# Kernel tuning notes

Hardware: AMD Instinct MI355X
Metric: run time of the kernel (lower is better)

Reference implementation:

```python
import jax, jax.numpy as jnp
import numpy as np

N, E, F, FE, H, R = 100000, 3200000, 2, 7, 64, 500
BN_EPS = 1e-5
LEAKY_SLOPE = 0.01


def _bn(h, g, b):
    # BatchNorm1d in training mode: batch statistics over the node axis
    m = h.mean(0)
    v = h.var(0)
    return (h - m) * jax.lax.rsqrt(v + BN_EPS) * g + b


def _gine_conv(x, src, dst, edge_attr, eps, el_w, el_b, w1, b1, g, bt, w2, b2):
    # message: relu(x_j + Lin(edge_attr)); aggregate: scatter-add at dst
    msg = jax.nn.relu(x[src] + edge_attr @ el_w + el_b)          # [E, d]
    agg = jax.ops.segment_sum(msg, dst, num_segments=N)          # [N, d]
    h = (1.0 + eps) * x + agg
    # nn: Linear -> BN -> ReLU -> Linear -> ReLU
    h = jax.nn.relu(_bn(h @ w1 + b1, g, bt))
    return jax.nn.relu(h @ w2 + b2)


def setup_inputs() -> dict:
    key = jax.random.key(0)
    ks = jax.random.split(key, 16)
    r = lambda k, s, sc=0.1: jax.random.normal(k, s, dtype=jnp.float32) * sc
    return {
        "x": jax.random.normal(ks[0], (N, F), dtype=jnp.float32),
        "edge_attr": jax.random.normal(ks[1], (E, FE), dtype=jnp.float32),
        "edge_index": jax.random.randint(ks[2], (2, E), 0, N),
        "epoch": 1,
        "eps1": jnp.zeros((), jnp.float32),
        "el1_w": r(ks[3], (FE, F)), "el1_b": jnp.zeros((F,), jnp.float32),
        "n1_w1": r(ks[4], (F, H)), "n1_b1": jnp.zeros((H,), jnp.float32),
        "n1_g": jnp.ones((H,), jnp.float32), "n1_bt": jnp.zeros((H,), jnp.float32),
        "n1_w2": r(ks[5], (H, H)), "n1_b2": jnp.zeros((H,), jnp.float32),
        "eps2": jnp.zeros((), jnp.float32),
        "el2_w": r(ks[6], (FE, H)), "el2_b": jnp.zeros((H,), jnp.float32),
        "n2_w1": r(ks[7], (H, H)), "n2_b1": jnp.zeros((H,), jnp.float32),
        "n2_g": jnp.ones((H,), jnp.float32), "n2_bt": jnp.zeros((H,), jnp.float32),
        "n2_w2": r(ks[8], (H, H)), "n2_b2": jnp.zeros((H,), jnp.float32),
        "reg_w": r(ks[9], (H, R)), "reg_b": jnp.zeros((R,), jnp.float32),
        "end_w": r(ks[10], (R, 1)), "end_b": jnp.zeros((1,), jnp.float32),
    }


def reference(x, edge_attr, edge_index, epoch,
              eps1, el1_w, el1_b, n1_w1, n1_b1, n1_g, n1_bt, n1_w2, n1_b2,
              eps2, el2_w, el2_b, n2_w1, n2_b1, n2_g, n2_bt, n2_w2, n2_b2,
              reg_w, reg_b, end_w, end_b):
    src, dst = edge_index[0], edge_index[1]
    out = _gine_conv(x, src, dst, edge_attr, eps1, el1_w, el1_b,
                     n1_w1, n1_b1, n1_g, n1_bt, n1_w2, n1_b2)
    for _ in range(3 - 1):  # num_layers=3, shared conv2 weights
        out = _gine_conv(out, src, dst, edge_attr, eps2, el2_w, el2_b,
                         n2_w1, n2_b1, n2_g, n2_bt, n2_w2, n2_b2)
    # dropout p=0.0 -> identity; epoch only resets dropout, no effect here
    out = out @ reg_w + reg_b
    out = jnp.where(out >= 0, out, LEAKY_SLOPE * out)  # LeakyReLU
    out = out @ end_w + end_b                            # [N, 1]
    return out
```

## Files before the change

kernel.cpp:

```cpp
#include <hip/hip_runtime.h>

#define NN 100000
#define NE 3200000

__global__ __launch_bounds__(256) void count_kernel(const int* __restrict__ dst,
                                                    int* __restrict__ cnt) {
  int stride = gridDim.x * 256;
  for (int e = blockIdx.x * 256 + threadIdx.x; e < NE; e += stride)
    atomicAdd(&cnt[dst[e]], 1);
}

__global__ __launch_bounds__(1024) void scan_kernel(const int* __restrict__ cnt,
                                                    int* __restrict__ rowptr,
                                                    int* __restrict__ ofs) {
  __shared__ int bsum[1024];
  int tid = threadIdx.x;
  const int CH = (NN + 1023) / 1024;
  int lo = tid * CH, hi = lo + CH < NN ? lo + CH : NN;
  if (lo > NN) lo = NN;
  if (hi < lo) hi = lo;
  int s = 0;
  for (int i = lo; i < hi; i++) s += cnt[i];
  bsum[tid] = s;
  __syncthreads();
  for (int off = 1; off < 1024; off <<= 1) {
    int v = bsum[tid];
    int u = (tid >= off) ? bsum[tid - off] : 0;
    __syncthreads();
    bsum[tid] = v + u;
    __syncthreads();
  }
  int pre = (tid == 0) ? 0 : bsum[tid - 1];
  for (int i = lo; i < hi; i++) {
    int cv = cnt[i];
    rowptr[i] = pre;
    ofs[i] = pre;
    pre += cv;
  }
  if (tid == 1023) rowptr[NN] = pre;
}

__global__ __launch_bounds__(256) void scatter2p_kernel(
    const int* __restrict__ src, const int* __restrict__ dst,
    const float* __restrict__ ea, int* __restrict__ ofs,
    float* __restrict__ pe, const float* __restrict__ x,
    const float* __restrict__ elw, const float* __restrict__ elb,
    float* __restrict__ msg1) {
  float w0[7], w1r[7];
#pragma unroll
  for (int k = 0; k < 7; k++) { w0[k] = elw[k * 2]; w1r[k] = elw[k * 2 + 1]; }
  float b0 = elb[0], b1 = elb[1];
  int stride = gridDim.x * 256;
  for (int e = blockIdx.x * 256 + threadIdx.x; e < NE; e += stride) {
    int sn = src[e];
    int pos = atomicAdd(&ofs[dst[e]], 1);
    float av[7];
#pragma unroll
    for (int k = 0; k < 7; k++) av[k] = ea[e * 7 + k];
    float4 a, b;
    a.x = av[0]; a.y = av[1]; a.z = av[2]; a.w = av[3];
    b.x = av[4]; b.y = av[5]; b.z = av[6];
    b.w = __int_as_float(sn);
    ((float4*)pe)[pos * 2 + 0] = a;
    ((float4*)pe)[pos * 2 + 1] = b;
    float m0 = b0, m1 = b1;
#pragma unroll
    for (int k = 0; k < 7; k++) {
      m0 = fmaf(av[k], w0[k], m0);
      m1 = fmaf(av[k], w1r[k], m1);
    }
    m0 = fmaxf(m0 + x[sn * 2 + 0], 0.f);
    m1 = fmaxf(m1 + x[sn * 2 + 1], 0.f);
    float2 mv; mv.x = m0; mv.y = m1;
    ((float2*)msg1)[pos] = mv;
  }
}

__global__ __launch_bounds__(256) void scatter1_kernel(
    const int* __restrict__ dst, int* __restrict__ ofs, int* __restrict__ eid_s) {
  int stride = gridDim.x * 256;
  for (int e = blockIdx.x * 256 + threadIdx.x; e < NE; e += stride) {
    int pos = atomicAdd(&ofs[dst[e]], 1);
    eid_s[pos] = e;
  }
}

__global__ __launch_bounds__(256) void l1sum_kernel(
    const int* __restrict__ rowptr, const float* __restrict__ msg1,
    float* __restrict__ agg) {
  int stride = gridDim.x * 256;
  for (int n = blockIdx.x * 256 + threadIdx.x; n < NN; n += stride) {
    int r0 = rowptr[n], r1 = rowptr[n + 1];
    float a0 = 0.f, a1 = 0.f;
    const float2* mp = (const float2*)msg1;
    for (int i = r0; i < r1; i++) {
      float2 v = mp[i];
      a0 += v.x;
      a1 += v.y;
    }
    agg[n * 2 + 0] = a0;
    agg[n * 2 + 1] = a1;
  }
}

__global__ __launch_bounds__(256) void l1agg_kernel(
    const int* __restrict__ rowptr, const int* __restrict__ eid_s,
    const int* __restrict__ src, const float* __restrict__ ea,
    const float* __restrict__ x, const float* __restrict__ elw,
    const float* __restrict__ elb, float* __restrict__ agg) {
  float w0[7], w1r[7];
#pragma unroll
  for (int k = 0; k < 7; k++) { w0[k] = elw[k * 2]; w1r[k] = elw[k * 2 + 1]; }
  float b0 = elb[0], b1 = elb[1];
  int stride = gridDim.x * 256;
  for (int n = blockIdx.x * 256 + threadIdx.x; n < NN; n += stride) {
    int r0 = rowptr[n], r1 = rowptr[n + 1];
    float a0 = 0.f, a1 = 0.f;
    for (int i = r0; i < r1; i++) {
      int e = eid_s[i];
      int sn = src[e];
      float m0 = b0, m1 = b1;
#pragma unroll
      for (int k = 0; k < 7; k++) {
        float a = ea[e * 7 + k];
        m0 = fmaf(a, w0[k], m0);
        m1 = fmaf(a, w1r[k], m1);
      }
      m0 = fmaxf(m0 + x[sn * 2 + 0], 0.f);
      m1 = fmaxf(m1 + x[sn * 2 + 1], 0.f);
      a0 += m0; a1 += m1;
    }
    agg[n * 2 + 0] = a0;
    agg[n * 2 + 1] = a1;
  }
}

__global__ __launch_bounds__(256) void gine64p_kernel(
    const int* __restrict__ rowptr, const float* __restrict__ edat,
    const float* __restrict__ xin, const float* __restrict__ elw,
    const float* __restrict__ elb, const float* __restrict__ w1,
    const float* __restrict__ b1, const float* __restrict__ eps_p,
    float* __restrict__ tbuf, float* __restrict__ stats) {
  __shared__ float wl[64 * 64];
  __shared__ float hb[4][64];
  __shared__ float red[256];
  int tid = threadIdx.x, lane = tid & 63, wv = tid >> 6;
  for (int i = tid; i < 64 * 64; i += 256) wl[i] = w1[i];
  float wel[7];
#pragma unroll
  for (int k = 0; k < 7; k++) wel[k] = elw[k * 64 + lane];
  float bel = elb[lane], b1c = b1[lane];
  float ep = 1.0f + *eps_p;
  float s = 0.f, ss = 0.f;
  __syncthreads();
  const float4* pe = (const float4*)edat;
  int nw = gridDim.x * 4;
  for (int n = blockIdx.x * 4 + wv; n < NN; n += nw) {
    int r0 = rowptr[n], r1 = rowptr[n + 1];
    float acc = 0.f;
    int i = r0;
    int rem = r1 - r0;
    if (rem >= 4) {
      float4 a0 = pe[2 * i + 0], b0 = pe[2 * i + 1];
      float4 a1 = pe[2 * i + 2], b1v = pe[2 * i + 3];
      float4 a2 = pe[2 * i + 4], b2 = pe[2 * i + 5];
      float4 a3 = pe[2 * i + 6], b3 = pe[2 * i + 7];
      while (true) {
        float g0 = xin[__float_as_int(b0.w) * 64 + lane];
        float g1 = xin[__float_as_int(b1v.w) * 64 + lane];
        float g2 = xin[__float_as_int(b2.w) * 64 + lane];
        float g3 = xin[__float_as_int(b3.w) * 64 + lane];
        i += 4; rem -= 4;
        bool more = rem >= 4;
        int ip = more ? i : r0;
        float4 na0 = pe[2 * ip + 0], nb0 = pe[2 * ip + 1];
        float4 na1 = pe[2 * ip + 2], nb1 = pe[2 * ip + 3];
        float4 na2 = pe[2 * ip + 4], nb2 = pe[2 * ip + 5];
        float4 na3 = pe[2 * ip + 6], nb3 = pe[2 * ip + 7];
        float m0 = bel, m1 = bel, m2 = bel, m3 = bel;
        m0 = fmaf(a0.x, wel[0], m0); m0 = fmaf(a0.y, wel[1], m0);
        m0 = fmaf(a0.z, wel[2], m0); m0 = fmaf(a0.w, wel[3], m0);
        m0 = fmaf(b0.x, wel[4], m0); m0 = fmaf(b0.y, wel[5], m0);
        m0 = fmaf(b0.z, wel[6], m0);
        m1 = fmaf(a1.x, wel[0], m1); m1 = fmaf(a1.y, wel[1], m1);
        m1 = fmaf(a1.z, wel[2], m1); m1 = fmaf(a1.w, wel[3], m1);
        m1 = fmaf(b1v.x, wel[4], m1); m1 = fmaf(b1v.y, wel[5], m1);
        m1 = fmaf(b1v.z, wel[6], m1);
        m2 = fmaf(a2.x, wel[0], m2); m2 = fmaf(a2.y, wel[1], m2);
        m2 = fmaf(a2.z, wel[2], m2); m2 = fmaf(a2.w, wel[3], m2);
        m2 = fmaf(b2.x, wel[4], m2); m2 = fmaf(b2.y, wel[5], m2);
        m2 = fmaf(b2.z, wel[6], m2);
        m3 = fmaf(a3.x, wel[0], m3); m3 = fmaf(a3.y, wel[1], m3);
        m3 = fmaf(a3.z, wel[2], m3); m3 = fmaf(a3.w, wel[3], m3);
        m3 = fmaf(b3.x, wel[4], m3); m3 = fmaf(b3.y, wel[5], m3);
        m3 = fmaf(b3.z, wel[6], m3);
        acc += fmaxf(m0 + g0, 0.f);
        acc += fmaxf(m1 + g1, 0.f);
        acc += fmaxf(m2 + g2, 0.f);
        acc += fmaxf(m3 + g3, 0.f);
        a0 = na0; b0 = nb0; a1 = na1; b1v = nb1;
        a2 = na2; b2 = nb2; a3 = na3; b3 = nb3;
        if (!more) break;
      }
    }
    for (; i < r1; i++) {
      float4 pa = pe[i * 2], pb = pe[i * 2 + 1];
      float m = bel;
      m = fmaf(pa.x, wel[0], m); m = fmaf(pa.y, wel[1], m);
      m = fmaf(pa.z, wel[2], m); m = fmaf(pa.w, wel[3], m);
      m = fmaf(pb.x, wel[4], m); m = fmaf(pb.y, wel[5], m);
      m = fmaf(pb.z, wel[6], m);
      m += xin[__float_as_int(pb.w) * 64 + lane];
      acc += fmaxf(m, 0.f);
    }
    float h = ep * xin[n * 64 + lane] + acc;
    hb[wv][lane] = h;
    float t = b1c;
#pragma unroll
    for (int k = 0; k < 64; k++) t = fmaf(hb[wv][k], wl[k * 64 + lane], t);
    tbuf[n * 64 + lane] = t;
    s += t;
    ss += t * t;
  }
  double* dsum = (double*)stats;
  red[tid] = s;
  __syncthreads();
  if (tid < 64) unsafeAtomicAdd(&dsum[tid], (double)(red[tid] + red[tid + 64] + red[tid + 128] + red[tid + 192]));
  __syncthreads();
  red[tid] = ss;
  __syncthreads();
  if (tid < 64) unsafeAtomicAdd(&dsum[64 + tid], (double)(red[tid] + red[tid + 64] + red[tid + 128] + red[tid + 192]));
}

__global__ __launch_bounds__(256) void gine64s_kernel(
    const int* __restrict__ rowptr, const int* __restrict__ eid_s,
    const int* __restrict__ src, const float* __restrict__ ea,
    const float* __restrict__ xin, const float* __restrict__ elw,
    const float* __restrict__ elb, const float* __restrict__ w1,
    const float* __restrict__ b1, const float* __restrict__ eps_p,
    float* __restrict__ tbuf, float* __restrict__ stats) {
  __shared__ float wl[64 * 64];
  __shared__ float hb[4][64];
  __shared__ float red[256];
  int tid = threadIdx.x, lane = tid & 63, wv = tid >> 6;
  for (int i = tid; i < 64 * 64; i += 256) wl[i] = w1[i];
  float wel[7];
#pragma unroll
  for (int k = 0; k < 7; k++) wel[k] = elw[k * 64 + lane];
  float bel = elb[lane], b1c = b1[lane];
  float ep = 1.0f + *eps_p;
  float s = 0.f, ss = 0.f;
  __syncthreads();
  int nw = gridDim.x * 4;
  for (int n = blockIdx.x * 4 + wv; n < NN; n += nw) {
    int r0 = rowptr[n], r1 = rowptr[n + 1];
    float acc = 0.f;
    for (int i = r0; i < r1; i++) {
      int e = eid_s[i];
      int sn = src[e];
      float m = bel;
#pragma unroll
      for (int k = 0; k < 7; k++) m = fmaf(ea[e * 7 + k], wel[k], m);
      m += xin[sn * 64 + lane];
      acc += fmaxf(m, 0.f);
    }
    float h = ep * xin[n * 64 + lane] + acc;
    hb[wv][lane] = h;
    float t = b1c;
#pragma unroll
    for (int k = 0; k < 64; k++) t = fmaf(hb[wv][k], wl[k * 64 + lane], t);
    tbuf[n * 64 + lane] = t;
    s += t;
    ss += t * t;
  }
  double* dsum = (double*)stats;
  red[tid] = s;
  __syncthreads();
  if (tid < 64) unsafeAtomicAdd(&dsum[tid], (double)(red[tid] + red[tid + 64] + red[tid + 128] + red[tid + 192]));
  __syncthreads();
  red[tid] = ss;
  __syncthreads();
  if (tid < 64) unsafeAtomicAdd(&dsum[64 + tid], (double)(red[tid] + red[tid + 64] + red[tid + 128] + red[tid + 192]));
}

__global__ __launch_bounds__(256) void edge1_kernel(
    const float* __restrict__ x, const float* __restrict__ ea,
    const int* __restrict__ src, const int* __restrict__ dst,
    const float* __restrict__ elw, const float* __restrict__ elb,
    float* __restrict__ agg) {
  float w0[7], w1[7];
#pragma unroll
  for (int k = 0; k < 7; k++) { w0[k] = elw[k * 2]; w1[k] = elw[k * 2 + 1]; }
  float b0 = elb[0], b1 = elb[1];
  int stride = gridDim.x * 256;
  for (int e = blockIdx.x * 256 + threadIdx.x; e < NE; e += stride) {
    int s = src[e], d = dst[e];
    float m0 = b0, m1 = b1;
#pragma unroll
    for (int k = 0; k < 7; k++) {
      float a = ea[e * 7 + k];
      m0 = fmaf(a, w0[k], m0);
      m1 = fmaf(a, w1[k], m1);
    }
    m0 = fmaxf(m0 + x[s * 2 + 0], 0.f);
    m1 = fmaxf(m1 + x[s * 2 + 1], 0.f);
    unsafeAtomicAdd(&agg[d * 2 + 0], m0);
    unsafeAtomicAdd(&agg[d * 2 + 1], m1);
  }
}

__global__ __launch_bounds__(256) void edge64_kernel(
    const float* __restrict__ xin, const float* __restrict__ ea,
    const int* __restrict__ src, const int* __restrict__ dst,
    const float* __restrict__ elw, const float* __restrict__ elb,
    float* __restrict__ agg) {
  int lane = threadIdx.x & 63;
  int wid = (blockIdx.x * 256 + threadIdx.x) >> 6;
  int nw = (gridDim.x * 256) >> 6;
  float w[7];
#pragma unroll
  for (int k = 0; k < 7; k++) w[k] = elw[k * 64 + lane];
  float b = elb[lane];
  for (int e = wid; e < NE; e += nw) {
    int eu = __builtin_amdgcn_readfirstlane(e);
    int s = src[eu];
    int d = dst[eu];
    float m = b;
#pragma unroll
    for (int k = 0; k < 7; k++) m = fmaf(ea[eu * 7 + k], w[k], m);
    m += xin[s * 64 + lane];
    m = fmaxf(m, 0.f);
    unsafeAtomicAdd(&agg[d * 64 + lane], m);
  }
}

__global__ __launch_bounds__(256) void nodeA64_kernel(
    const float* __restrict__ xin, float* __restrict__ tbuf,
    const float* __restrict__ w1, const float* __restrict__ b1,
    const float* __restrict__ eps_p, float* __restrict__ stats) {
  __shared__ float wl[64 * 64];
  __shared__ float hbuf[4][64];
  __shared__ float red[256];
  int tid = threadIdx.x;
  int c = tid & 63, nl = tid >> 6;
  for (int i = tid; i < 64 * 64; i += 256) wl[i] = w1[i];
  float ep = 1.0f + *eps_p;
  float bc = b1[c];
  float s = 0.f, ss = 0.f;
  __syncthreads();
  for (int n0 = blockIdx.x * 4; n0 < NN; n0 += gridDim.x * 4) {
    int n = n0 + nl;
    bool valid = n < NN;
    float h = 0.f;
    if (valid) h = ep * xin[n * 64 + c] + tbuf[n * 64 + c];
    hbuf[nl][c] = h;
    __syncthreads();
    if (valid) {
      float t = bc;
#pragma unroll
      for (int k = 0; k < 64; k++) t = fmaf(hbuf[nl][k], wl[k * 64 + c], t);
      tbuf[n * 64 + c] = t;
      s += t;
      ss += t * t;
    }
    __syncthreads();
  }
  double* dsum = (double*)stats;
  red[tid] = s;
  __syncthreads();
  if (tid < 64) unsafeAtomicAdd(&dsum[tid], (double)(red[tid] + red[tid + 64] + red[tid + 128] + red[tid + 192]));
  __syncthreads();
  red[tid] = ss;
  __syncthreads();
  if (tid < 64) unsafeAtomicAdd(&dsum[64 + tid], (double)(red[tid] + red[tid + 64] + red[tid + 128] + red[tid + 192]));
}

__global__ __launch_bounds__(256) void nodeA2_kernel(
    const float* __restrict__ x, const float* __restrict__ agg1,
    float* __restrict__ tbuf, const float* __restrict__ w1,
    const float* __restrict__ b1, const float* __restrict__ eps_p,
    float* __restrict__ stats) {
  __shared__ float red[256];
  int tid = threadIdx.x;
  int c = tid & 63, nl = tid >> 6;
  float wa = w1[c], wb = w1[64 + c], bc = b1[c];
  float ep = 1.0f + *eps_p;
  float s = 0.f, ss = 0.f;
  for (int n0 = blockIdx.x * 4; n0 < NN; n0 += gridDim.x * 4) {
    int n = n0 + nl;
    if (n < NN) {
      float h0 = ep * x[n * 2 + 0] + agg1[n * 2 + 0];
      float h1 = ep * x[n * 2 + 1] + agg1[n * 2 + 1];
      float t = fmaf(h1, wb, fmaf(h0, wa, bc));
      tbuf[n * 64 + c] = t;
      s += t;
      ss += t * t;
    }
  }
  double* dsum = (double*)stats;
  red[tid] = s;
  __syncthreads();
  if (tid < 64) unsafeAtomicAdd(&dsum[tid], (double)(red[tid] + red[tid + 64] + red[tid + 128] + red[tid + 192]));
  __syncthreads();
  red[tid] = ss;
  __syncthreads();
  if (tid < 64) unsafeAtomicAdd(&dsum[64 + tid], (double)(red[tid] + red[tid + 64] + red[tid + 128] + red[tid + 192]));
}

__global__ void statsfin_kernel(float* stats, const float* __restrict__ g,
                                const float* __restrict__ bt) {
  int c = threadIdx.x;
  const double* ds = (const double*)stats;
  double m = ds[c] / (double)NN;
  double v = ds[64 + c] / (double)NN - m * m;
  float sc = g[c] * (float)(1.0 / sqrt(v + 1e-5));
  stats[256 + c] = sc;
  stats[320 + c] = bt[c] - (float)m * sc;
}

__global__ __launch_bounds__(256) void nodeB_kernel(
    const float* __restrict__ tin, float* __restrict__ outb,
    const float* __restrict__ w2, const float* __restrict__ b2,
    const float* __restrict__ stats) {
  __shared__ float wl[64 * 64];
  __shared__ float ubuf[4][64];
  int tid = threadIdx.x;
  int c = tid & 63, nl = tid >> 6;
  for (int i = tid; i < 64 * 64; i += 256) wl[i] = w2[i];
  float scale = stats[256 + c], shift = stats[320 + c], bc = b2[c];
  __syncthreads();
  for (int n0 = blockIdx.x * 4; n0 < NN; n0 += gridDim.x * 4) {
    int n = n0 + nl;
    bool valid = n < NN;
    float u = 0.f;
    if (valid) {
      float t = tin[n * 64 + c];
      u = fmaxf(fmaf(t, scale, shift), 0.f);
    }
    ubuf[nl][c] = u;
    __syncthreads();
    if (valid) {
      float o = bc;
#pragma unroll
      for (int k = 0; k < 64; k++) o = fmaf(ubuf[nl][k], wl[k * 64 + c], o);
      outb[n * 64 + c] = fmaxf(o, 0.f);
    }
    __syncthreads();
  }
}

__global__ __launch_bounds__(256) void final_kernel(
    const float* __restrict__ xin, const float* __restrict__ regw,
    const float* __restrict__ regb, const float* __restrict__ endw,
    const float* __restrict__ endb, float* __restrict__ out) {
  __shared__ float wl[64 * 128];
  __shared__ float eb[256];
  int tid = threadIdx.x;
  int node = blockIdx.x * 256 + tid;
  bool valid = node < NN;
  float xr[64];
  if (valid) {
    const float4* xp = (const float4*)(xin + node * 64);
#pragma unroll
    for (int k4 = 0; k4 < 16; k4++) {
      float4 v = xp[k4];
      xr[k4 * 4 + 0] = v.x; xr[k4 * 4 + 1] = v.y;
      xr[k4 * 4 + 2] = v.z; xr[k4 * 4 + 3] = v.w;
    }
  }
  float y = 0.f;
  for (int ch = 0; ch < 4; ch++) {
    int j0 = ch * 125;
    __syncthreads();
    for (int idx = tid; idx < 64 * 125; idx += 256) {
      int k = idx / 125;
      int jl = idx - k * 125;
      wl[k * 128 + jl] = regw[k * 500 + j0 + jl];
    }
    if (tid < 125) { eb[tid] = regb[j0 + tid]; eb[128 + tid] = endw[j0 + tid]; }
    __syncthreads();
    if (valid) {
      int jl = 0;
      for (; jl + 4 <= 125; jl += 4) {
        float t0 = eb[jl], t1 = eb[jl + 1], t2 = eb[jl + 2], t3 = eb[jl + 3];
#pragma unroll
        for (int k = 0; k < 64; k++) {
          float4 w4 = *(const float4*)&wl[k * 128 + jl];
          float xv = xr[k];
          t0 = fmaf(xv, w4.x, t0);
          t1 = fmaf(xv, w4.y, t1);
          t2 = fmaf(xv, w4.z, t2);
          t3 = fmaf(xv, w4.w, t3);
        }
        t0 = t0 >= 0.f ? t0 : 0.01f * t0;
        t1 = t1 >= 0.f ? t1 : 0.01f * t1;
        t2 = t2 >= 0.f ? t2 : 0.01f * t2;
        t3 = t3 >= 0.f ? t3 : 0.01f * t3;
        y += t0 * eb[128 + jl] + t1 * eb[128 + jl + 1] + t2 * eb[128 + jl + 2] + t3 * eb[128 + jl + 3];
      }
      {
        float t = eb[124];
#pragma unroll
        for (int k = 0; k < 64; k++) t = fmaf(xr[k], wl[k * 128 + 124], t);
        t = t >= 0.f ? t : 0.01f * t;
        y += t * eb[128 + 124];
      }
    }
  }
  if (valid) out[node] = y + endb[0];
}

extern "C" void kernel_launch(void* const* d_in, const int* in_sizes, int n_in,
                              void* d_out, int out_size, void* d_ws, size_t ws_size,
                              hipStream_t stream) {
  const float* x    = (const float*)d_in[0];
  const float* ea   = (const float*)d_in[1];
  const int*   ei   = (const int*)d_in[2];
  const float* eps1 = (const float*)d_in[4];
  const float* el1w = (const float*)d_in[5];
  const float* el1b = (const float*)d_in[6];
  const float* n1w1 = (const float*)d_in[7];
  const float* n1b1 = (const float*)d_in[8];
  const float* n1g  = (const float*)d_in[9];
  const float* n1bt = (const float*)d_in[10];
  const float* n1w2 = (const float*)d_in[11];
  const float* n1b2 = (const float*)d_in[12];
  const float* eps2 = (const float*)d_in[13];
  const float* el2w = (const float*)d_in[14];
  const float* el2b = (const float*)d_in[15];
  const float* n2w1 = (const float*)d_in[16];
  const float* n2b1 = (const float*)d_in[17];
  const float* n2g  = (const float*)d_in[18];
  const float* n2bt = (const float*)d_in[19];
  const float* n2w2 = (const float*)d_in[20];
  const float* n2b2 = (const float*)d_in[21];
  const float* regw = (const float*)d_in[22];
  const float* regb = (const float*)d_in[23];
  const float* endw = (const float*)d_in[24];
  const float* endb = (const float*)d_in[25];
  const int* srcp = ei;
  const int* dstp = ei + NE;

  const size_t o_stats  = 0;
  const size_t o_rowptr = 512;
  const size_t o_cnt    = 100516;
  const size_t o_buf0   = 200576;
  const size_t o_buf1   = 6600576;
  const size_t o_agg1   = 13000576;
  const size_t o_edat   = 13200576;
  const size_t needA2 = (o_edat + (size_t)NE * 8) * 4;
  const size_t needA1 = (o_edat + (size_t)NE) * 4;
  const size_t needB  = (2 * 6600000 + 384) * 4;

  float* wsf = (float*)d_ws;

  if (ws_size >= needA1) {
    const bool packed = ws_size >= needA2;
    float* stats = wsf + o_stats;
    int* rowptr  = (int*)(wsf + o_rowptr);
    int* cnt     = (int*)(wsf + o_cnt);
    float* buf0  = wsf + o_buf0;
    float* buf1  = wsf + o_buf1;
    float* agg1  = wsf + o_agg1;
    float* edat  = wsf + o_edat;
    float* msg1  = buf0;

    hipMemsetAsync(cnt, 0, NN * sizeof(int), stream);
    count_kernel<<<4096, 256, 0, stream>>>(dstp, cnt);
    scan_kernel<<<1, 1024, 0, stream>>>(cnt, rowptr, cnt);
    if (packed)
      scatter2p_kernel<<<4096, 256, 0, stream>>>(srcp, dstp, ea, cnt, edat,
                                                 x, el1w, el1b, msg1);
    else
      scatter1_kernel<<<4096, 256, 0, stream>>>(dstp, cnt, (int*)edat);

    hipMemsetAsync(stats, 0, 128 * sizeof(double), stream);
    if (packed)
      l1sum_kernel<<<391, 256, 0, stream>>>(rowptr, msg1, agg1);
    else
      l1agg_kernel<<<391, 256, 0, stream>>>(rowptr, (const int*)edat, srcp, ea,
                                            x, el1w, el1b, agg1);
    nodeA2_kernel<<<2048, 256, 0, stream>>>(x, agg1, buf1, n1w1, n1b1, eps1, stats);
    statsfin_kernel<<<1, 64, 0, stream>>>(stats, n1g, n1bt);
    nodeB_kernel<<<2048, 256, 0, stream>>>(buf1, buf1, n1w2, n1b2, stats);

    float* cur = buf1;
    float* wrk = buf0;
    for (int l = 0; l < 2; l++) {
      hipMemsetAsync(stats, 0, 128 * sizeof(double), stream);
      if (packed)
        gine64p_kernel<<<4096, 256, 0, stream>>>(rowptr, edat, cur, el2w, el2b,
                                                 n2w1, n2b1, eps2, wrk, stats);
      else
        gine64s_kernel<<<4096, 256, 0, stream>>>(rowptr, (const int*)edat, srcp,
                                                 ea, cur, el2w, el2b, n2w1, n2b1,
                                                 eps2, wrk, stats);
      statsfin_kernel<<<1, 64, 0, stream>>>(stats, n2g, n2bt);
      nodeB_kernel<<<2048, 256, 0, stream>>>(wrk, wrk, n2w2, n2b2, stats);
      float* tmp = cur; cur = wrk; wrk = tmp;
    }

    final_kernel<<<(NN + 255) / 256, 256, 0, stream>>>(cur, regw, regb, endw, endb,
                                                       (float*)d_out);
    return;
  }

  if (ws_size < needB) return;
  const size_t BUF = 6600000;
  float* buf0 = (float*)d_ws;
  float* buf1 = buf0 + BUF;
  float* stats = buf1 + BUF;

  float* t1 = buf1;
  float* agg1 = buf1 + NN * 64;
  hipMemsetAsync(agg1, 0, NN * 2 * sizeof(float), stream);
  hipMemsetAsync(stats, 0, 128 * sizeof(double), stream);
  edge1_kernel<<<2048, 256, 0, stream>>>(x, ea, srcp, dstp, el1w, el1b, agg1);
  nodeA2_kernel<<<2048, 256, 0, stream>>>(x, agg1, t1, n1w1, n1b1, eps1, stats);
  statsfin_kernel<<<1, 64, 0, stream>>>(stats, n1g, n1bt);
  nodeB_kernel<<<2048, 256, 0, stream>>>(t1, buf1, n1w2, n1b2, stats);

  float* cur = buf1;
  float* wrk = buf0;
  for (int l = 0; l < 2; l++) {
    hipMemsetAsync(wrk, 0, NN * 64 * sizeof(float), stream);
    hipMemsetAsync(stats, 0, 128 * sizeof(double), stream);
    edge64_kernel<<<2048, 256, 0, stream>>>(cur, ea, srcp, dstp, el2w, el2b, wrk);
    nodeA64_kernel<<<2048, 256, 0, stream>>>(cur, wrk, n2w1, n2b1, eps2, stats);
    statsfin_kernel<<<1, 64, 0, stream>>>(stats, n2g, n2bt);
    nodeB_kernel<<<2048, 256, 0, stream>>>(wrk, wrk, n2w2, n2b2, stats);
    float* tmp = cur; cur = wrk; wrk = tmp;
  }

  final_kernel<<<(NN + 255) / 256, 256, 0, stream>>>(cur, regw, regb, endw, endb,
                                                     (float*)d_out);
}
```

Measured before the change: 1.535 ms.

## Split edge scatter into permutation plus gather-pack, and batch 8 gathers per node

The single atomic scatter kernel, which wrote packed edge data to random positions, is replaced by two passes. First a scatter writes only edge ids into a permutation. Then a pack kernel reads through that permutation and writes the packed edge records and layer-1 messages sequentially. The layer-2/3 aggregation kernel now loads 8 source ids first and issues 8 independent feature gathers before computing, so more memory requests are in flight at once. The tail is handled by padding with the node's own row, and the workspace requirement grows slightly to cover over-reads past the last record. The cost is an extra kernel launch and random reads of the edge attributes in place of random writes.

```diff
diff --git a/kernel.cpp b/kernel.cpp
--- a/kernel.cpp
+++ b/kernel.cpp
@@ -40,48 +40,47 @@
   if (tid == 1023) rowptr[NN] = pre;
 }
 
-__global__ __launch_bounds__(256) void scatter2p_kernel(
-    const int* __restrict__ src, const int* __restrict__ dst,
-    const float* __restrict__ ea, int* __restrict__ ofs,
-    float* __restrict__ pe, const float* __restrict__ x,
-    const float* __restrict__ elw, const float* __restrict__ elb,
-    float* __restrict__ msg1) {
-  float w0[7], w1r[7];
-#pragma unroll
-  for (int k = 0; k < 7; k++) { w0[k] = elw[k * 2]; w1r[k] = elw[k * 2 + 1]; }
-  float b0 = elb[0], b1 = elb[1];
-  int stride = gridDim.x * 256;
-  for (int e = blockIdx.x * 256 + threadIdx.x; e < NE; e += stride) {
-    int sn = src[e];
-    int pos = atomicAdd(&ofs[dst[e]], 1);
-    float av[7];
-#pragma unroll
-    for (int k = 0; k < 7; k++) av[k] = ea[e * 7 + k];
-    float4 a, b;
-    a.x = av[0]; a.y = av[1]; a.z = av[2]; a.w = av[3];
-    b.x = av[4]; b.y = av[5]; b.z = av[6];
-    b.w = __int_as_float(sn);
-    ((float4*)pe)[pos * 2 + 0] = a;
-    ((float4*)pe)[pos * 2 + 1] = b;
-    float m0 = b0, m1 = b1;
-#pragma unroll
-    for (int k = 0; k < 7; k++) {
-      m0 = fmaf(av[k], w0[k], m0);
-      m1 = fmaf(av[k], w1r[k], m1);
-    }
-    m0 = fmaxf(m0 + x[sn * 2 + 0], 0.f);
-    m1 = fmaxf(m1 + x[sn * 2 + 1], 0.f);
-    float2 mv; mv.x = m0; mv.y = m1;
-    ((float2*)msg1)[pos] = mv;
-  }
-}
-
 __global__ __launch_bounds__(256) void scatter1_kernel(
     const int* __restrict__ dst, int* __restrict__ ofs, int* __restrict__ eid_s) {
   int stride = gridDim.x * 256;
   for (int e = blockIdx.x * 256 + threadIdx.x; e < NE; e += stride) {
     int pos = atomicAdd(&ofs[dst[e]], 1);
     eid_s[pos] = e;
+  }
+}
+
+__global__ __launch_bounds__(256) void pack_kernel(
+    const int* __restrict__ perm, const int* __restrict__ src,
+    const float* __restrict__ ea, const float* __restrict__ x,
+    const float* __restrict__ elw, const float* __restrict__ elb,
+    float* __restrict__ pe, float* __restrict__ msg1) {
+  float w0[7], w1r[7];
+#pragma unroll
+  for (int k = 0; k < 7; k++) { w0[k] = elw[k * 2]; w1r[k] = elw[k * 2 + 1]; }
+  float b0 = elb[0], b1 = elb[1];
+  int stride = gridDim.x * 256;
+  for (int i = blockIdx.x * 256 + threadIdx.x; i < NE; i += stride) {
+    int e = perm[i];
+    int sn = src[e];
+    float av[7];
+#pragma unroll
+    for (int k = 0; k < 7; k++) av[k] = ea[e * 7 + k];
+    float4 a, b;
+    a.x = av[0]; a.y = av[1]; a.z = av[2]; a.w = av[3];
+    b.x = av[4]; b.y = av[5]; b.z = av[6];
+    b.w = __int_as_float(sn);
+    ((float4*)pe)[i * 2 + 0] = a;
+    ((float4*)pe)[i * 2 + 1] = b;
+    float m0 = b0, m1 = b1;
+#pragma unroll
+    for (int k = 0; k < 7; k++) {
+      m0 = fmaf(av[k], w0[k], m0);
+      m1 = fmaf(av[k], w1r[k], m1);
+    }
+    m0 = fmaxf(m0 + x[sn * 2 + 0], 0.f);
+    m1 = fmaxf(m1 + x[sn * 2 + 1], 0.f);
+    float2 mv; mv.x = m0; mv.y = m1;
+    ((float2*)msg1)[i] = mv;
   }
 }
 
@@ -135,7 +134,7 @@
   }
 }
 
-__global__ __launch_bounds__(256) void gine64p_kernel(
+__global__ __launch_bounds__(256) void gine64q_kernel(
     const int* __restrict__ rowptr, const float* __restrict__ edat,
     const float* __restrict__ xin, const float* __restrict__ elw,
     const float* __restrict__ elb, const float* __restrict__ w1,
@@ -153,65 +152,60 @@
   float ep = 1.0f + *eps_p;
   float s = 0.f, ss = 0.f;
   __syncthreads();
-  const float4* pe = (const float4*)edat;
+  const float* pf = edat;
+  const float4* p4 = (const float4*)edat;
+  const float2* p2 = (const float2*)edat;
+  const float* xl = xin + lane;
   int nw = gridDim.x * 4;
   for (int n = blockIdx.x * 4 + wv; n < NN; n += nw) {
     int r0 = rowptr[n], r1 = rowptr[n + 1];
     float acc = 0.f;
     int i = r0;
-    int rem = r1 - r0;
-    if (rem >= 4) {
-      float4 a0 = pe[2 * i + 0], b0 = pe[2 * i + 1];
-      float4 a1 = pe[2 * i + 2], b1v = pe[2 * i + 3];
-      float4 a2 = pe[2 * i + 4], b2 = pe[2 * i + 5];
-      float4 a3 = pe[2 * i + 6], b3 = pe[2 * i + 7];
-      while (true) {
-        float g0 = xin[__float_as_int(b0.w) * 64 + lane];
-        float g1 = xin[__float_as_int(b1v.w) * 64 + lane];
-        float g2 = xin[__float_as_int(b2.w) * 64 + lane];
-        float g3 = xin[__float_as_int(b3.w) * 64 + lane];
-        i += 4; rem -= 4;
-        bool more = rem >= 4;
-        int ip = more ? i : r0;
-        float4 na0 = pe[2 * ip + 0], nb0 = pe[2 * ip + 1];
-        float4 na1 = pe[2 * ip + 2], nb1 = pe[2 * ip + 3];
-        float4 na2 = pe[2 * ip + 4], nb2 = pe[2 * ip + 5];
-        float4 na3 = pe[2 * ip + 6], nb3 = pe[2 * ip + 7];
-        float m0 = bel, m1 = bel, m2 = bel, m3 = bel;
-        m0 = fmaf(a0.x, wel[0], m0); m0 = fmaf(a0.y, wel[1], m0);
-        m0 = fmaf(a0.z, wel[2], m0); m0 = fmaf(a0.w, wel[3], m0);
-        m0 = fmaf(b0.x, wel[4], m0); m0 = fmaf(b0.y, wel[5], m0);
-        m0 = fmaf(b0.z, wel[6], m0);
-        m1 = fmaf(a1.x, wel[0], m1); m1 = fmaf(a1.y, wel[1], m1);
-        m1 = fmaf(a1.z, wel[2], m1); m1 = fmaf(a1.w, wel[3], m1);
-        m1 = fmaf(b1v.x, wel[4], m1); m1 = fmaf(b1v.y, wel[5], m1);
-        m1 = fmaf(b1v.z, wel[6], m1);
-        m2 = fmaf(a2.x, wel[0], m2); m2 = fmaf(a2.y, wel[1], m2);
-        m2 = fmaf(a2.z, wel[2], m2); m2 = fmaf(a2.w, wel[3], m2);
-        m2 = fmaf(b2.x, wel[4], m2); m2 = fmaf(b2.y, wel[5], m2);
-        m2 = fmaf(b2.z, wel[6], m2);
-        m3 = fmaf(a3.x, wel[0], m3); m3 = fmaf(a3.y, wel[1], m3);
-        m3 = fmaf(a3.z, wel[2], m3); m3 = fmaf(a3.w, wel[3], m3);
-        m3 = fmaf(b3.x, wel[4], m3); m3 = fmaf(b3.y, wel[5], m3);
-        m3 = fmaf(b3.z, wel[6], m3);
-        acc += fmaxf(m0 + g0, 0.f);
-        acc += fmaxf(m1 + g1, 0.f);
-        acc += fmaxf(m2 + g2, 0.f);
-        acc += fmaxf(m3 + g3, 0.f);
-        a0 = na0; b0 = nb0; a1 = na1; b1v = nb1;
-        a2 = na2; b2 = nb2; a3 = na3; b3 = nb3;
-        if (!more) break;
+    while (i + 8 <= r1) {
+      int sid[8];
+#pragma unroll
+      for (int j = 0; j < 8; j++) sid[j] = __float_as_int(pf[(i + j) * 8 + 7]);
+      float g[8];
+#pragma unroll
+      for (int j = 0; j < 8; j++) g[j] = xl[sid[j] * 64];
+#pragma unroll
+      for (int j = 0; j < 8; j++) {
+        float4 a = p4[(i + j) * 2];
+        float2 b2 = p2[(i + j) * 4 + 2];
+        float c6 = pf[(i + j) * 8 + 6];
+        float m = bel;
+        m = fmaf(a.x, wel[0], m); m = fmaf(a.y, wel[1], m);
+        m = fmaf(a.z, wel[2], m); m = fmaf(a.w, wel[3], m);
+        m = fmaf(b2.x, wel[4], m); m = fmaf(b2.y, wel[5], m);
+        m = fmaf(c6, wel[6], m);
+        acc += fmaxf(m + g[j], 0.f);
       }
-    }
-    for (; i < r1; i++) {
-      float4 pa = pe[i * 2], pb = pe[i * 2 + 1];
-      float m = bel;
-      m = fmaf(pa.x, wel[0], m); m = fmaf(pa.y, wel[1], m);
-      m = fmaf(pa.z, wel[2], m); m = fmaf(pa.w, wel[3], m);
-      m = fmaf(pb.x, wel[4], m); m = fmaf(pb.y, wel[5], m);
-      m = fmaf(pb.z, wel[6], m);
-      m += xin[__float_as_int(pb.w) * 64 + lane];
-      acc += fmaxf(m, 0.f);
+      i += 8;
+    }
+    if (i < r1) {
+      int cnt = r1 - i;
+      int sid[8];
+#pragma unroll
+      for (int j = 0; j < 8; j++) {
+        int raw = __float_as_int(pf[(i + j) * 8 + 7]);
+        sid[j] = (j < cnt) ? raw : n;
+      }
+      float g[8];
+#pragma unroll
+      for (int j = 0; j < 8; j++) g[j] = xl[sid[j] * 64];
+#pragma unroll
+      for (int j = 0; j < 8; j++) {
+        float4 a = p4[(i + j) * 2];
+        float2 b2 = p2[(i + j) * 4 + 2];
+        float c6 = pf[(i + j) * 8 + 6];
+        float m = bel;
+        m = fmaf(a.x, wel[0], m); m = fmaf(a.y, wel[1], m);
+        m = fmaf(a.z, wel[2], m); m = fmaf(a.w, wel[3], m);
+        m = fmaf(b2.x, wel[4], m); m = fmaf(b2.y, wel[5], m);
+        m = fmaf(c6, wel[6], m);
+        float v = fmaxf(m + g[j], 0.f);
+        acc += (j < cnt) ? v : 0.f;
+      }
     }
     float h = ep * xin[n * 64 + lane] + acc;
     hb[wv][lane] = h;
@@ -548,7 +542,7 @@
   const size_t o_buf1   = 6600576;
   const size_t o_agg1   = 13000576;
   const size_t o_edat   = 13200576;
-  const size_t needA2 = (o_edat + (size_t)NE * 8) * 4;
+  const size_t needA2 = (o_edat + (size_t)NE * 8 + 64) * 4;
   const size_t needA1 = (o_edat + (size_t)NE) * 4;
   const size_t needB  = (2 * 6600000 + 384) * 4;
 
@@ -564,15 +558,18 @@
     float* agg1  = wsf + o_agg1;
     float* edat  = wsf + o_edat;
     float* msg1  = buf0;
+    int*   perm  = (int*)buf1;
 
     hipMemsetAsync(cnt, 0, NN * sizeof(int), stream);
     count_kernel<<<4096, 256, 0, stream>>>(dstp, cnt);
     scan_kernel<<<1, 1024, 0, stream>>>(cnt, rowptr, cnt);
-    if (packed)
-      scatter2p_kernel<<<4096, 256, 0, stream>>>(srcp, dstp, ea, cnt, edat,
-                                                 x, el1w, el1b, msg1);
-    else
+    if (packed) {
+      scatter1_kernel<<<4096, 256, 0, stream>>>(dstp, cnt, perm);
+      pack_kernel<<<4096, 256, 0, stream>>>(perm, srcp, ea, x, el1w, el1b,
+                                            edat, msg1);
+    } else {
       scatter1_kernel<<<4096, 256, 0, stream>>>(dstp, cnt, (int*)edat);
+    }
 
     hipMemsetAsync(stats, 0, 128 * sizeof(double), stream);
     if (packed)
@@ -589,7 +586,7 @@
     for (int l = 0; l < 2; l++) {
       hipMemsetAsync(stats, 0, 128 * sizeof(double), stream);
       if (packed)
-        gine64p_kernel<<<4096, 256, 0, stream>>>(rowptr, edat, cur, el2w, el2b,
+        gine64q_kernel<<<4096, 256, 0, stream>>>(rowptr, edat, cur, el2w, el2b,
                                                  n2w1, n2b1, eps2, wrk, stats);
       else
         gine64s_kernel<<<4096, 256, 0, stream>>>(rowptr, (const int*)edat, srcp,
```

Measured after the change: 2.047 ms. 33.4% more time.

## Software-pipeline edge gathers two groups ahead and fold BN finalize into nodeB

Applied to the files above, without the earlier changes.

Rewrites the layer-2/3 edge aggregation loop so packed edge records are loaded two groups of four ahead and the source-feature gathers one group ahead, with a masked tail instead of a scalar remainder loop. Out-of-range source ids from padding are clamped to zero so the speculative loads stay safe. The workspace requirement grows slightly to cover the overread. The separate BN statistics finalize kernel is removed, and every nodeB block recomputes scale and shift from the double sums, saving three launches at the cost of redundant per-block work.

```diff
diff --git a/kernel.cpp b/kernel.cpp
--- a/kernel.cpp
+++ b/kernel.cpp
@@ -135,7 +135,24 @@
   }
 }
 
-__global__ __launch_bounds__(256) void gine64p_kernel(
+#define PROJ(m, aq, bq) do { \
+  m = bel; \
+  m = fmaf((aq).x, wel[0], m); m = fmaf((aq).y, wel[1], m); \
+  m = fmaf((aq).z, wel[2], m); m = fmaf((aq).w, wel[3], m); \
+  m = fmaf((bq).x, wel[4], m); m = fmaf((bq).y, wel[5], m); \
+  m = fmaf((bq).z, wel[6], m); } while (0)
+
+#define LOADG(base) do { \
+  na0 = p4[2 * (base) + 0]; nb0 = p4[2 * (base) + 1]; \
+  na1 = p4[2 * (base) + 2]; nb1 = p4[2 * (base) + 3]; \
+  na2 = p4[2 * (base) + 4]; nb2 = p4[2 * (base) + 5]; \
+  na3 = p4[2 * (base) + 6]; nb3 = p4[2 * (base) + 7]; } while (0)
+
+#define CLAMPSID(dst, bq) do { \
+  unsigned raw = (unsigned)__float_as_int((bq).w); \
+  dst = (raw >= (unsigned)NN) ? 0u : raw; } while (0)
+
+__global__ __launch_bounds__(256) void gine64r_kernel(
     const int* __restrict__ rowptr, const float* __restrict__ edat,
     const float* __restrict__ xin, const float* __restrict__ elw,
     const float* __restrict__ elb, const float* __restrict__ w1,
@@ -145,7 +162,7 @@
   __shared__ float hb[4][64];
   __shared__ float red[256];
   int tid = threadIdx.x, lane = tid & 63, wv = tid >> 6;
-  for (int i = tid; i < 64 * 64; i += 256) wl[i] = w1[i];
+  for (int i2 = tid; i2 < 64 * 64; i2 += 256) wl[i2] = w1[i2];
   float wel[7];
 #pragma unroll
   for (int k = 0; k < 7; k++) wel[k] = elw[k * 64 + lane];
@@ -153,65 +170,46 @@
   float ep = 1.0f + *eps_p;
   float s = 0.f, ss = 0.f;
   __syncthreads();
-  const float4* pe = (const float4*)edat;
+  const float4* p4 = (const float4*)edat;
+  const float* xl = xin + lane;
   int nw = gridDim.x * 4;
   for (int n = blockIdx.x * 4 + wv; n < NN; n += nw) {
     int r0 = rowptr[n], r1 = rowptr[n + 1];
+    int len = r1 - r0;
     float acc = 0.f;
-    int i = r0;
-    int rem = r1 - r0;
-    if (rem >= 4) {
-      float4 a0 = pe[2 * i + 0], b0 = pe[2 * i + 1];
-      float4 a1 = pe[2 * i + 2], b1v = pe[2 * i + 3];
-      float4 a2 = pe[2 * i + 4], b2 = pe[2 * i + 5];
-      float4 a3 = pe[2 * i + 6], b3 = pe[2 * i + 7];
-      while (true) {
-        float g0 = xin[__float_as_int(b0.w) * 64 + lane];
-        float g1 = xin[__float_as_int(b1v.w) * 64 + lane];
-        float g2 = xin[__float_as_int(b2.w) * 64 + lane];
-        float g3 = xin[__float_as_int(b3.w) * 64 + lane];
-        i += 4; rem -= 4;
-        bool more = rem >= 4;
-        int ip = more ? i : r0;
-        float4 na0 = pe[2 * ip + 0], nb0 = pe[2 * ip + 1];
-        float4 na1 = pe[2 * ip + 2], nb1 = pe[2 * ip + 3];
-        float4 na2 = pe[2 * ip + 4], nb2 = pe[2 * ip + 5];
-        float4 na3 = pe[2 * ip + 6], nb3 = pe[2 * ip + 7];
-        float m0 = bel, m1 = bel, m2 = bel, m3 = bel;
-        m0 = fmaf(a0.x, wel[0], m0); m0 = fmaf(a0.y, wel[1], m0);
-        m0 = fmaf(a0.z, wel[2], m0); m0 = fmaf(a0.w, wel[3], m0);
-        m0 = fmaf(b0.x, wel[4], m0); m0 = fmaf(b0.y, wel[5], m0);
-        m0 = fmaf(b0.z, wel[6], m0);
-        m1 = fmaf(a1.x, wel[0], m1); m1 = fmaf(a1.y, wel[1], m1);
-        m1 = fmaf(a1.z, wel[2], m1); m1 = fmaf(a1.w, wel[3], m1);
-        m1 = fmaf(b1v.x, wel[4], m1); m1 = fmaf(b1v.y, wel[5], m1);
-        m1 = fmaf(b1v.z, wel[6], m1);
-        m2 = fmaf(a2.x, wel[0], m2); m2 = fmaf(a2.y, wel[1], m2);
-        m2 = fmaf(a2.z, wel[2], m2); m2 = fmaf(a2.w, wel[3], m2);
-        m2 = fmaf(b2.x, wel[4], m2); m2 = fmaf(b2.y, wel[5], m2);
-        m2 = fmaf(b2.z, wel[6], m2);
-        m3 = fmaf(a3.x, wel[0], m3); m3 = fmaf(a3.y, wel[1], m3);
-        m3 = fmaf(a3.z, wel[2], m3); m3 = fmaf(a3.w, wel[3], m3);
-        m3 = fmaf(b3.x, wel[4], m3); m3 = fmaf(b3.y, wel[5], m3);
-        m3 = fmaf(b3.z, wel[6], m3);
-        acc += fmaxf(m0 + g0, 0.f);
-        acc += fmaxf(m1 + g1, 0.f);
-        acc += fmaxf(m2 + g2, 0.f);
-        acc += fmaxf(m3 + g3, 0.f);
-        a0 = na0; b0 = nb0; a1 = na1; b1v = nb1;
-        a2 = na2; b2 = nb2; a3 = na3; b3 = nb3;
-        if (!more) break;
+    if (len > 0) {
+      int ng = (len + 3) >> 2;
+      float4 na0, nb0, na1, nb1, na2, nb2, na3, nb3;
+      LOADG(r0);
+      float4 ca0 = na0, cb0 = nb0, ca1 = na1, cb1 = nb1;
+      float4 ca2 = na2, cb2 = nb2, ca3 = na3, cb3 = nb3;
+      int b1i = (ng > 1) ? (r0 + 4) : r0;
+      LOADG(b1i);
+      float mc0, mc1, mc2, mc3;
+      PROJ(mc0, ca0, cb0); PROJ(mc1, ca1, cb1);
+      PROJ(mc2, ca2, cb2); PROJ(mc3, ca3, cb3);
+      unsigned s0, s1, s2, s3;
+      CLAMPSID(s0, cb0); CLAMPSID(s1, cb1); CLAMPSID(s2, cb2); CLAMPSID(s3, cb3);
+      float gc0 = xl[s0 * 64], gc1 = xl[s1 * 64];
+      float gc2 = xl[s2 * 64], gc3 = xl[s3 * 64];
+      for (int g = 0; g < ng; g++) {
+        float mn0, mn1, mn2, mn3;
+        PROJ(mn0, na0, nb0); PROJ(mn1, na1, nb1);
+        PROJ(mn2, na2, nb2); PROJ(mn3, na3, nb3);
+        unsigned t0, t1, t2, t3;
+        CLAMPSID(t0, nb0); CLAMPSID(t1, nb1); CLAMPSID(t2, nb2); CLAMPSID(t3, nb3);
+        float gn0 = xl[t0 * 64], gn1 = xl[t1 * 64];
+        float gn2 = xl[t2 * 64], gn3 = xl[t3 * 64];
+        int b2 = (g + 2 < ng) ? (r0 + 4 * (g + 2)) : r0;
+        LOADG(b2);
+        int rem = len - 4 * g;
+        acc += (rem > 0) ? fmaxf(mc0 + gc0, 0.f) : 0.f;
+        acc += (rem > 1) ? fmaxf(mc1 + gc1, 0.f) : 0.f;
+        acc += (rem > 2) ? fmaxf(mc2 + gc2, 0.f) : 0.f;
+        acc += (rem > 3) ? fmaxf(mc3 + gc3, 0.f) : 0.f;
+        mc0 = mn0; mc1 = mn1; mc2 = mn2; mc3 = mn3;
+        gc0 = gn0; gc1 = gn1; gc2 = gn2; gc3 = gn3;
       }
-    }
-    for (; i < r1; i++) {
-      float4 pa = pe[i * 2], pb = pe[i * 2 + 1];
-      float m = bel;
-      m = fmaf(pa.x, wel[0], m); m = fmaf(pa.y, wel[1], m);
-      m = fmaf(pa.z, wel[2], m); m = fmaf(pa.w, wel[3], m);
-      m = fmaf(pb.x, wel[4], m); m = fmaf(pb.y, wel[5], m);
-      m = fmaf(pb.z, wel[6], m);
-      m += xin[__float_as_int(pb.w) * 64 + lane];
-      acc += fmaxf(m, 0.f);
     }
     float h = ep * xin[n * 64 + lane] + acc;
     hb[wv][lane] = h;
@@ -407,28 +405,28 @@
   if (tid < 64) unsafeAtomicAdd(&dsum[64 + tid], (double)(red[tid] + red[tid + 64] + red[tid + 128] + red[tid + 192]));
 }
 
-__global__ void statsfin_kernel(float* stats, const float* __restrict__ g,
-                                const float* __restrict__ bt) {
-  int c = threadIdx.x;
-  const double* ds = (const double*)stats;
-  double m = ds[c] / (double)NN;
-  double v = ds[64 + c] / (double)NN - m * m;
-  float sc = g[c] * (float)(1.0 / sqrt(v + 1e-5));
-  stats[256 + c] = sc;
-  stats[320 + c] = bt[c] - (float)m * sc;
-}
-
 __global__ __launch_bounds__(256) void nodeB_kernel(
     const float* __restrict__ tin, float* __restrict__ outb,
     const float* __restrict__ w2, const float* __restrict__ b2,
-    const float* __restrict__ stats) {
+    const float* __restrict__ stats, const float* __restrict__ g,
+    const float* __restrict__ bt) {
   __shared__ float wl[64 * 64];
   __shared__ float ubuf[4][64];
+  __shared__ float scsh[128];
   int tid = threadIdx.x;
   int c = tid & 63, nl = tid >> 6;
   for (int i = tid; i < 64 * 64; i += 256) wl[i] = w2[i];
-  float scale = stats[256 + c], shift = stats[320 + c], bc = b2[c];
-  __syncthreads();
+  if (tid < 64) {
+    const double* ds = (const double*)stats;
+    double m = ds[tid] / (double)NN;
+    double v = ds[64 + tid] / (double)NN - m * m;
+    float sc = g[tid] * (float)(1.0 / sqrt(v + 1e-5));
+    scsh[tid] = sc;
+    scsh[64 + tid] = bt[tid] - (float)m * sc;
+  }
+  float bc = b2[c];
+  __syncthreads();
+  float scale = scsh[c], shift = scsh[64 + c];
   for (int n0 = blockIdx.x * 4; n0 < NN; n0 += gridDim.x * 4) {
     int n = n0 + nl;
     bool valid = n < NN;
@@ -548,7 +546,7 @@
   const size_t o_buf1   = 6600576;
   const size_t o_agg1   = 13000576;
   const size_t o_edat   = 13200576;
-  const size_t needA2 = (o_edat + (size_t)NE * 8) * 4;
+  const size_t needA2 = (o_edat + (size_t)NE * 8 + 96) * 4;
   const size_t needA1 = (o_edat + (size_t)NE) * 4;
   const size_t needB  = (2 * 6600000 + 384) * 4;
 
@@ -581,22 +579,20 @@
       l1agg_kernel<<<391, 256, 0, stream>>>(rowptr, (const int*)edat, srcp, ea,
                                             x, el1w, el1b, agg1);
     nodeA2_kernel<<<2048, 256, 0, stream>>>(x, agg1, buf1, n1w1, n1b1, eps1, stats);
-    statsfin_kernel<<<1, 64, 0, stream>>>(stats, n1g, n1bt);
-    nodeB_kernel<<<2048, 256, 0, stream>>>(buf1, buf1, n1w2, n1b2, stats);
+    nodeB_kernel<<<2048, 256, 0, stream>>>(buf1, buf1, n1w2, n1b2, stats, n1g, n1bt);
 
     float* cur = buf1;
     float* wrk = buf0;
     for (int l = 0; l < 2; l++) {
       hipMemsetAsync(stats, 0, 128 * sizeof(double), stream);
       if (packed)
-        gine64p_kernel<<<4096, 256, 0, stream>>>(rowptr, edat, cur, el2w, el2b,
+        gine64r_kernel<<<4096, 256, 0, stream>>>(rowptr, edat, cur, el2w, el2b,
                                                  n2w1, n2b1, eps2, wrk, stats);
       else
         gine64s_kernel<<<4096, 256, 0, stream>>>(rowptr, (const int*)edat, srcp,
                                                  ea, cur, el2w, el2b, n2w1, n2b1,
                                                  eps2, wrk, stats);
-      statsfin_kernel<<<1, 64, 0, stream>>>(stats, n2g, n2bt);
-      nodeB_kernel<<<2048, 256, 0, stream>>>(wrk, wrk, n2w2, n2b2, stats);
+      nodeB_kernel<<<2048, 256, 0, stream>>>(wrk, wrk, n2w2, n2b2, stats, n2g, n2bt);
       float* tmp = cur; cur = wrk; wrk = tmp;
     }
 
@@ -617,8 +613,7 @@
   hipMemsetAsync(stats, 0, 128 * sizeof(double), stream);
   edge1_kernel<<<2048, 256, 0, stream>>>(x, ea, srcp, dstp, el1w, el1b, agg1);
   nodeA2_kernel<<<2048, 256, 0, stream>>>(x, agg1, t1, n1w1, n1b1, eps1, stats);
-  statsfin_kernel<<<1, 64, 0, stream>>>(stats, n1g, n1bt);
-  nodeB_kernel<<<2048, 256, 0, stream>>>(t1, buf1, n1w2, n1b2, stats);
+  nodeB_kernel<<<2048, 256, 0, stream>>>(t1, buf1, n1w2, n1b2, stats, n1g, n1bt);
 
   float* cur = buf1;
   float* wrk = buf0;
@@ -627,8 +622,7 @@
     hipMemsetAsync(stats, 0, 128 * sizeof(double), stream);
     edge64_kernel<<<2048, 256, 0, stream>>>(cur, ea, srcp, dstp, el2w, el2b, wrk);
     nodeA64_kernel<<<2048, 256, 0, stream>>>(cur, wrk, n2w1, n2b1, eps2, stats);
-    statsfin_kernel<<<1, 64, 0, stream>>>(stats, n2g, n2bt);
-    nodeB_kernel<<<2048, 256, 0, stream>>>(wrk, wrk, n2w2, n2b2, stats);
+    nodeB_kernel<<<2048, 256, 0, stream>>>(wrk, wrk, n2w2, n2b2, stats, n2g, n2bt);
     float* tmp = cur; cur = wrk; wrk = tmp;
   }
 
```

Measured after the change: 1.539 ms. Within noise of the previous version (+0.3%).
